# Optimization experiments

Measured on AMD Instinct MI355X. Metric: run time of the kernel, lower is better.

Reference implementation:

```python
import jax, jax.numpy as jnp
import numpy as np
from jax import lax

H, D_INNER, G, D_GATE, K, DH = 2560, 8192, 32, 4096, 4, 128
EPS = 1e-6


def setup_inputs() -> dict:
    key = jax.random.key(0)
    ks = jax.random.split(key, 9)
    B, L = 2, 4096
    s = 0.02
    return {
        "hidden_states": jax.random.normal(ks[0], (B, L, H), jnp.float32),
        "W_qkv": jax.random.normal(ks[1], (D_INNER, H), jnp.float32) * s,
        "W_b": jax.random.normal(ks[2], (G, H), jnp.float32) * s,
        "W_a": jax.random.normal(ks[3], (G, H), jnp.float32) * s,
        "conv_w": jax.random.normal(ks[4], (D_INNER, 1, K), jnp.float32) * s,
        "W_out": jax.random.normal(ks[5], (H, D_GATE), jnp.float32) * s,
        "norm_w": jnp.ones((DH,), jnp.float32),
        "A_log": jax.random.normal(ks[6], (G,), jnp.float32) * 0.1,
        "dt_bias": jax.random.normal(ks[7], (G,), jnp.float32) * 0.1,
    }


def _ssm_scan(x, B_coeff, C_coeff, A_log, dt_bias):
    # x: [B,L,G,DH], B_coeff/C_coeff: [B,L,G]
    A = -jnp.exp(A_log.astype(jnp.float32))          # [G]
    dt = jax.nn.softplus(dt_bias.astype(jnp.float32))  # [G]
    dA = jnp.exp(dt * A)                              # [G], time-invariant decay
    xf = x.astype(jnp.float32).transpose(1, 0, 2, 3)      # [L,B,G,DH]
    Bf = B_coeff.astype(jnp.float32).transpose(1, 0, 2)   # [L,B,G]
    Cf = C_coeff.astype(jnp.float32).transpose(1, 0, 2)
    h0 = jnp.zeros(x.shape[0:1] + (G, DH), jnp.float32)   # [B,G,DH]

    def step(h, inp):
        x_t, b_t, c_t = inp
        h = dA[None, :, None] * h + (dt * b_t)[..., None] * x_t
        return h, c_t[..., None] * h

    _, ys = lax.scan(step, h0, (xf, Bf, Cf))  # ys: [L,B,G,DH]
    return ys.transpose(1, 0, 2, 3).astype(x.dtype)


def reference(hidden_states, W_qkv, W_b, W_a, conv_w, W_out, norm_w, A_log, dt_bias):
    Bsz, L, _ = hidden_states.shape
    xz = hidden_states @ W_qkv.T           # [B,L,8192]
    B_coeff = hidden_states @ W_b.T        # [B,L,32]
    C_coeff = hidden_states @ W_a.T        # [B,L,32]
    # causal depthwise conv1d (padding K-1 on left, right pad trimmed)
    xz_c = lax.conv_general_dilated(
        xz.transpose(0, 2, 1), conv_w, (1,), [(K - 1, 0)],
        feature_group_count=D_INNER,
        dimension_numbers=("NCH", "OIH", "NCH"))
    xz_c = xz_c.transpose(0, 2, 1)          # [B,L,8192]
    x, z_inner = jnp.split(xz_c, 2, axis=-1)  # each [B,L,4096]
    x = jax.nn.silu(x).reshape(Bsz, L, G, DH)
    y = _ssm_scan(x, B_coeff, C_coeff, A_log, dt_bias)  # [B,L,G,DH]
    # RMSNorm over head_dim
    y = y * lax.rsqrt(jnp.mean(y * y, axis=-1, keepdims=True) + EPS) * norm_w
    y = y.reshape(Bsz, L, D_GATE) * jax.nn.silu(z_inner)
    return y @ W_out.T                      # [B,L,2560]
```

## Files before the change

### kernel.cpp

```cpp
#include <hip/hip_runtime.h>
#include <cstdint>
#include <cstddef>

#define H_DIM   2560
#define DINNER  8192
#define GHEADS  32
#define DGATE   4096
#define DH      128
#define BSZ     2
#define LSEQ    4096
#define MROWS   (BSZ*LSEQ)
#define NXPAD   4352
#define NCHUNK  64
#define SCHUNK  (LSEQ/NCHUNK)

typedef __attribute__((ext_vector_type(4))) float    f32x4;
typedef __attribute__((ext_vector_type(8))) _Float16 f16x8;
typedef unsigned short u16;
typedef unsigned int   u32;

static __device__ __forceinline__ u16 f2h(float f) {
  _Float16 h = (_Float16)f;
  union { _Float16 h; u16 u; } v; v.h = h; return v.u;
}
static __device__ __forceinline__ float h2f(u16 u) {
  union { u16 u; _Float16 h; } v; v.u = u; return (float)v.h;
}
static __device__ __forceinline__ float silu(float x) {
  return x / (1.0f + expf(-x));
}

__global__ void cast_f32_f16(const float* __restrict__ in, u16* __restrict__ out, int n4) {
  int i = blockIdx.x * blockDim.x + threadIdx.x;
  if (i < n4) {
    f32x4 v = ((const f32x4*)in)[i];
    u32 p0 = (u32)f2h(v[0]) | ((u32)f2h(v[1]) << 16);
    u32 p1 = (u32)f2h(v[2]) | ((u32)f2h(v[3]) << 16);
    ((uint2*)out)[i] = make_uint2(p0, p1);
  }
}

__global__ void build_wc(const float* __restrict__ Wqkv, const float* __restrict__ Wb,
                         const float* __restrict__ Wa, u16* __restrict__ wcp,
                         u16* __restrict__ wz) {
  int row = blockIdx.x;
  if (row >= NXPAD) {
    const float* src = Wqkv + (size_t)(4096 + row - NXPAD) * H_DIM;
    u16* oh = wz + (size_t)(row - NXPAD) * H_DIM;
    for (int i = threadIdx.x; i < H_DIM / 4; i += blockDim.x) {
      f32x4 v = ((const f32x4*)src)[i];
      ((uint2*)oh)[i] = make_uint2((u32)f2h(v[0]) | ((u32)f2h(v[1]) << 16),
                                   (u32)f2h(v[2]) | ((u32)f2h(v[3]) << 16));
    }
    return;
  }
  const float* src = nullptr;
  if (row < 4096)              src = Wqkv + (size_t)row * H_DIM;
  else if (row < 4128)         src = Wb + (size_t)(row - 4096) * H_DIM;
  else if (row < 4160)         src = Wa + (size_t)(row - 4128) * H_DIM;
  u16* oh = wcp + (size_t)row * H_DIM;
  for (int i = threadIdx.x; i < H_DIM / 4; i += blockDim.x) {
    u32 p0 = 0, p1 = 0;
    if (src) {
      f32x4 v = ((const f32x4*)src)[i];
      p0 = (u32)f2h(v[0]) | ((u32)f2h(v[1]) << 16);
      p1 = (u32)f2h(v[2]) | ((u32)f2h(v[3]) << 16);
    }
    ((uint2*)oh)[i] = make_uint2(p0, p1);
  }
}

static __device__ __forceinline__ void gload16(const u16* g, u16* l) {
  __builtin_amdgcn_global_load_lds(
      (const __attribute__((address_space(1))) u32*)g,
      (__attribute__((address_space(3))) u32*)l, 16, 0, 0);
}

#define BAR()    asm volatile("s_barrier" ::: "memory")
#define WAITV3() asm volatile("s_waitcnt vmcnt(3)" ::: "memory")
#define WAITV0() asm volatile("s_waitcnt vmcnt(0)" ::: "memory")

template<bool OUT_F16>
__global__ __launch_bounds__(512)
void gemm_h(const u16* __restrict__ A, const u16* __restrict__ Bt,
            void* __restrict__ Cout, int K, int ldc, int nbx, int cpx) {
  __shared__ __align__(16) u16 As0[128 * 32];
  __shared__ __align__(16) u16 As1[128 * 32];
  __shared__ __align__(16) u16 Bs0[256 * 32];
  __shared__ __align__(16) u16 Bs1[256 * 32];
  const int tid  = threadIdx.x;
  const int lane = tid & 63;
  const int wave = tid >> 6;
  const int wm = (wave & 1) * 64;
  const int wn = (wave >> 1) * 64;
  const int bid = blockIdx.x;
  const int lsw = (bid & 7) * cpx + (bid >> 3);
  const int by  = lsw / nbx;
  const int bx  = lsw - by * nbx;
  const size_t bm = (size_t)by * 128;
  const size_t bn = (size_t)bx * 256;

  const int srow = tid >> 2;
  const int scol = (((tid & 3) ^ ((srow >> 1) & 3)) << 3);
  const u16* Ab = A + bm * (size_t)K;
  const u16* Bb = Bt + bn * (size_t)K;

  f32x4 acc[4][4];
#pragma unroll
  for (int i = 0; i < 4; i++)
#pragma unroll
    for (int j = 0; j < 4; j++) acc[i][j] = (f32x4){0.f, 0.f, 0.f, 0.f};

#define STAGE(AS, BS, kk)                                                \
  do {                                                                   \
    gload16(Ab + (size_t)srow * K + (kk) + scol, &AS[tid * 8]);          \
    gload16(Bb + (size_t)srow * K + (kk) + scol, &BS[tid * 8]);          \
    gload16(Bb + (size_t)(128 + srow) * K + (kk) + scol, &BS[4096 + tid * 8]); \
  } while (0)

#define COMPUTE(AS, BS)                                                           \
  do {                                                                            \
    const int fr = lane & 15;                                                     \
    const int fo = (((lane >> 4) ^ ((fr >> 1) & 3)) << 3);    \
    f16x8 av[4], bv[4];                                                           \
    _Pragma("unroll")                                                             \
    for (int i = 0; i < 4; i++) av[i] = *(const f16x8*)&AS[(wm + i * 16 + fr) * 32 + fo]; \
    _Pragma("unroll")                                                             \
    for (int j = 0; j < 4; j++) bv[j] = *(const f16x8*)&BS[(wn + j * 16 + fr) * 32 + fo]; \
    __builtin_amdgcn_s_setprio(1);                                                \
    _Pragma("unroll")                                                             \
    for (int i = 0; i < 4; i++)                                                   \
      _Pragma("unroll")                                                           \
      for (int j = 0; j < 4; j++)                                                 \
        acc[i][j] = __builtin_amdgcn_mfma_f32_16x16x32_f16(av[i], bv[j], acc[i][j], 0, 0, 0); \
    __builtin_amdgcn_s_setprio(0);                                                \
  } while (0)

  STAGE(As0, Bs0, 0);
  STAGE(As1, Bs1, 32);
  WAITV3();
  BAR();
  for (int k0 = 0; k0 < K; k0 += 64) {
    COMPUTE(As0, Bs0);
    BAR();
    if (k0 + 64 < K) { STAGE(As0, Bs0, k0 + 64); WAITV3(); }
    else             { WAITV0(); }
    BAR();
    COMPUTE(As1, Bs1);
    BAR();
    if (k0 + 96 < K) { STAGE(As1, Bs1, k0 + 96); WAITV3(); }
    else             { WAITV0(); }
    BAR();
  }
#undef STAGE
#undef COMPUTE

  const int cr = (lane >> 4) * 4, ccol = lane & 15;
#pragma unroll
  for (int i = 0; i < 4; i++)
#pragma unroll
    for (int j = 0; j < 4; j++)
#pragma unroll
      for (int r = 0; r < 4; r++) {
        size_t row = bm + wm + i * 16 + cr + r;
        size_t col = bn + wn + j * 16 + ccol;
        if (OUT_F16) ((u16*)Cout)[row * ldc + col] = f2h(acc[i][j][r]);
        else         ((float*)Cout)[row * ldc + col] = acc[i][j][r];
      }
}

__global__ __launch_bounds__(64)
void scan_pass1(const float* __restrict__ xzx, const float* __restrict__ conv_w,
                const float* __restrict__ A_log, const float* __restrict__ dt_bias,
                float* __restrict__ E) {
  const int bid = blockIdx.x;
  const int c   = bid & (NCHUNK - 1);
  const int bg  = bid >> 6;
  const int g   = bg & (GHEADS - 1);
  const int b   = bg >> 5;
  const int lane = threadIdx.x;
  const int ch0 = g * DH + lane, ch1 = ch0 + 64;

  const f32x4 w0 = ((const f32x4*)conv_w)[ch0];
  const f32x4 w1 = ((const f32x4*)conv_w)[ch1];
  const float dt = log1pf(expf(dt_bias[g]));
  const float Ac = -expf(A_log[g]);
  const float dA = expf(dt * Ac);

  const int l0 = c * SCHUNK;
  const float* base = xzx + (size_t)b * LSEQ * NXPAD;

  float xm3 = 0, xm2 = 0, xm1 = 0, Xm3 = 0, Xm2 = 0, Xm1 = 0;
#pragma unroll
  for (int j = 0; j < 3; j++) {
    int l = l0 - 3 + j;
    float v0 = 0, v1 = 0;
    if (l >= 0) {
      const float* rp = base + (size_t)l * NXPAD;
      v0 = rp[ch0]; v1 = rp[ch1];
    }
    if (j == 0) { xm3 = v0; Xm3 = v1; }
    else if (j == 1) { xm2 = v0; Xm2 = v1; }
    else { xm1 = v0; Xm1 = v1; }
  }
  float h0 = 0.f, h1 = 0.f;
  for (int t = 0; t < SCHUNK; t++) {
    const float* rp = base + (size_t)(l0 + t) * NXPAD;
    float xc0 = rp[ch0], xc1 = rp[ch1];
    float cx0 = w0[0] * xm3 + w0[1] * xm2 + w0[2] * xm1 + w0[3] * xc0;
    float cx1 = w1[0] * Xm3 + w1[1] * Xm2 + w1[2] * Xm1 + w1[3] * xc1;
    xm3 = xm2; xm2 = xm1; xm1 = xc0;
    Xm3 = Xm2; Xm2 = Xm1; Xm1 = xc1;
    float u = dt * rp[DGATE + g];
    h0 = dA * h0 + u * silu(cx0);
    h1 = dA * h1 + u * silu(cx1);
  }
  float* ep = E + (size_t)bid * DH;
  ep[lane] = h0; ep[lane + 64] = h1;
}

__global__ __launch_bounds__(64)
void scan_pass2(const float* __restrict__ E, float* __restrict__ Hs,
                const float* __restrict__ A_log, const float* __restrict__ dt_bias) {
  const int bg = blockIdx.x;
  const int g = bg & (GHEADS - 1);
  const int lane = threadIdx.x;
  const float dt = log1pf(expf(dt_bias[g]));
  const float Ac = -expf(A_log[g]);
  const float dAS = expf(dt * Ac * (float)SCHUNK);
  float h0 = 0.f, h1 = 0.f;
  for (int c = 0; c < NCHUNK; c++) {
    size_t idx = ((size_t)bg * NCHUNK + c) * DH;
    Hs[idx + lane] = h0; Hs[idx + lane + 64] = h1;
    h0 = dAS * h0 + E[idx + lane];
    h1 = dAS * h1 + E[idx + lane + 64];
  }
}

__global__ __launch_bounds__(64)
void scan_pass3(const float* __restrict__ xzx, const u16* __restrict__ xzz,
                const float* __restrict__ conv_w,
                const float* __restrict__ A_log, const float* __restrict__ dt_bias,
                const float* __restrict__ norm_w, const float* __restrict__ Hs,
                u16* __restrict__ gbuf) {
  const int bid = blockIdx.x;
  const int c   = bid & (NCHUNK - 1);
  const int bg  = bid >> 6;
  const int g   = bg & (GHEADS - 1);
  const int b   = bg >> 5;
  const int lane = threadIdx.x;
  const int ch0 = g * DH + lane, ch1 = ch0 + 64;

  const f32x4 wx0 = ((const f32x4*)conv_w)[ch0];
  const f32x4 wx1 = ((const f32x4*)conv_w)[ch1];
  const f32x4 wz0 = ((const f32x4*)conv_w)[DGATE + ch0];
  const f32x4 wz1 = ((const f32x4*)conv_w)[DGATE + ch1];
  const float nw0 = norm_w[lane], nw1 = norm_w[lane + 64];

  const float dt = log1pf(expf(dt_bias[g]));
  const float Ac = -expf(A_log[g]);
  const float dA = expf(dt * Ac);

  const int l0 = c * SCHUNK;
  const float* basex = xzx + (size_t)b * LSEQ * NXPAD;
  const u16*   basez = xzz + (size_t)b * LSEQ * DGATE;

  float xm3 = 0, xm2 = 0, xm1 = 0, Xm3 = 0, Xm2 = 0, Xm1 = 0;
  float zm3 = 0, zm2 = 0, zm1 = 0, Zm3 = 0, Zm2 = 0, Zm1 = 0;
#pragma unroll
  for (int j = 0; j < 3; j++) {
    int l = l0 - 3 + j;
    float vx0 = 0, vx1 = 0, vz0 = 0, vz1 = 0;
    if (l >= 0) {
      const float* rp = basex + (size_t)l * NXPAD;
      const u16*   rz = basez + (size_t)l * DGATE;
      vx0 = rp[ch0]; vx1 = rp[ch1];
      vz0 = h2f(rz[ch0]); vz1 = h2f(rz[ch1]);
    }
    if (j == 0) { xm3 = vx0; Xm3 = vx1; zm3 = vz0; Zm3 = vz1; }
    else if (j == 1) { xm2 = vx0; Xm2 = vx1; zm2 = vz0; Zm2 = vz1; }
    else { xm1 = vx0; Xm1 = vx1; zm1 = vz0; Zm1 = vz1; }
  }
  float h0 = Hs[(size_t)bid * DH + lane];
  float h1 = Hs[(size_t)bid * DH + lane + 64];
  for (int t = 0; t < SCHUNK; t++) {
    const int l = l0 + t;
    const float* rp = basex + (size_t)l * NXPAD;
    const u16*   rz = basez + (size_t)l * DGATE;
    float xc0 = rp[ch0], xc1 = rp[ch1];
    float zc0 = h2f(rz[ch0]), zc1 = h2f(rz[ch1]);
    float cx0 = wx0[0] * xm3 + wx0[1] * xm2 + wx0[2] * xm1 + wx0[3] * xc0;
    float cx1 = wx1[0] * Xm3 + wx1[1] * Xm2 + wx1[2] * Xm1 + wx1[3] * xc1;
    float cz0 = wz0[0] * zm3 + wz0[1] * zm2 + wz0[2] * zm1 + wz0[3] * zc0;
    float cz1 = wz1[0] * Zm3 + wz1[1] * Zm2 + wz1[2] * Zm1 + wz1[3] * zc1;
    xm3 = xm2; xm2 = xm1; xm1 = xc0;  Xm3 = Xm2; Xm2 = Xm1; Xm1 = xc1;
    zm3 = zm2; zm2 = zm1; zm1 = zc0;  Zm3 = Zm2; Zm2 = Zm1; Zm1 = zc1;
    float bcl = rp[DGATE + g];
    float ccl = rp[DGATE + 32 + g];
    float u = dt * bcl;
    h0 = dA * h0 + u * silu(cx0);
    h1 = dA * h1 + u * silu(cx1);
    float y0 = ccl * h0, y1 = ccl * h1;
    float ss = y0 * y0 + y1 * y1;
    ss += __shfl_xor(ss, 32); ss += __shfl_xor(ss, 16); ss += __shfl_xor(ss, 8);
    ss += __shfl_xor(ss, 4);  ss += __shfl_xor(ss, 2);  ss += __shfl_xor(ss, 1);
    const float sc = rsqrtf(ss * (1.0f / DH) + 1e-6f);
    u16* op = gbuf + (size_t)(b * LSEQ + l) * DGATE + g * DH;
    op[lane]      = f2h(y0 * sc * nw0 * silu(cz0));
    op[lane + 64] = f2h(y1 * sc * nw1 * silu(cz1));
  }
}

extern "C" void kernel_launch(void* const* d_in, const int* in_sizes, int n_in,
                              void* d_out, int out_size, void* d_ws, size_t ws_size,
                              hipStream_t stream) {
  (void)in_sizes; (void)n_in; (void)out_size; (void)ws_size;
  const float* hs    = (const float*)d_in[0];
  const float* Wqkv  = (const float*)d_in[1];
  const float* Wb    = (const float*)d_in[2];
  const float* Wa    = (const float*)d_in[3];
  const float* convw = (const float*)d_in[4];
  const float* Wout  = (const float*)d_in[5];
  const float* normw = (const float*)d_in[6];
  const float* Alog  = (const float*)d_in[7];
  const float* dtb   = (const float*)d_in[8];
  float* out = (float*)d_out;

  char* ws = (char*)d_ws;
  size_t off = 0;
  auto alloc = [&](size_t bytes) { void* p = ws + off; off += (bytes + 255) & ~(size_t)255; return p; };
  float* xzx    = (float*)alloc((size_t)MROWS * NXPAD * 4);
  u16*   xzz    = (u16*)alloc((size_t)MROWS * DGATE * 2);
  u16*   wcp    = (u16*)alloc((size_t)NXPAD * H_DIM * 2);
  u16*   wz     = (u16*)alloc((size_t)DGATE * H_DIM * 2);
  (void)alloc((size_t)24 << 20);
  u16*   wout_h = (u16*)alloc((size_t)H_DIM * DGATE * 2);
  float* E      = (float*)alloc((size_t)BSZ * GHEADS * NCHUNK * DH * 4);
  float* Hst    = (float*)alloc((size_t)BSZ * GHEADS * NCHUNK * DH * 4);
  u16*   gbuf   = wcp;
  u16*   hs_h   = (u16*)d_out;

  const int n4_hs = MROWS * H_DIM / 4;
  cast_f32_f16<<<(n4_hs + 255) / 256, 256, 0, stream>>>(hs, hs_h, n4_hs);
  build_wc<<<NXPAD + DGATE, 256, 0, stream>>>(Wqkv, Wb, Wa, wcp, wz);
  const int n4_wo = H_DIM * DGATE / 4;
  cast_f32_f16<<<(n4_wo + 255) / 256, 256, 0, stream>>>(Wout, wout_h, n4_wo);

  gemm_h<false><<<1088, 512, 0, stream>>>(hs_h, wcp, xzx, H_DIM, NXPAD, 17, 136);
  gemm_h<true><<<1024, 512, 0, stream>>>(hs_h, wz, xzz, H_DIM, DGATE, 16, 128);

  scan_pass1<<<BSZ * GHEADS * NCHUNK, 64, 0, stream>>>(xzx, convw, Alog, dtb, E);
  scan_pass2<<<BSZ * GHEADS, 64, 0, stream>>>(E, Hst, Alog, dtb);
  scan_pass3<<<BSZ * GHEADS * NCHUNK, 64, 0, stream>>>(xzx, xzz, convw, Alog, dtb, normw, Hst, gbuf);

  gemm_h<false><<<640, 512, 0, stream>>>(gbuf, wout_h, out, DGATE, H_DIM, 10, 80);
}
```

Before: 854.5 us.

## Merge input GEMMs into one launch with triple-buffered LDS pipeline

Concatenates the xz and z weight matrices into one combined fp16 buffer so the two input projection GEMMs run as a single launch, with each tile choosing an f32 or f16 output by column block. The GEMM mainloop moves from double to triple buffering of LDS stages, waiting on vmcnt(6) so more loads are in flight. The tile mapping is changed to column-major over 64 row blocks, and launch bounds now request 4 waves per SIMD. The cost is more LDS per block (72KB), which may reduce occupancy, and tail handling that assumes particular K multiples.

Result: slower. 1.482 ms (+73.4%).

```diff
diff --git a/kernel.cpp b/kernel.cpp
--- a/kernel.cpp
+++ b/kernel.cpp
@@ -11,6 +11,7 @@
 #define LSEQ    4096
 #define MROWS   (BSZ*LSEQ)
 #define NXPAD   4352
+#define NWCOMB  8448
 #define NCHUNK  64
 #define SCHUNK  (LSEQ/NCHUNK)
 
@@ -41,24 +42,14 @@
 }
 
 __global__ void build_wc(const float* __restrict__ Wqkv, const float* __restrict__ Wb,
-                         const float* __restrict__ Wa, u16* __restrict__ wcp,
-                         u16* __restrict__ wz) {
+                         const float* __restrict__ Wa, u16* __restrict__ wcomb) {
   int row = blockIdx.x;
-  if (row >= NXPAD) {
-    const float* src = Wqkv + (size_t)(4096 + row - NXPAD) * H_DIM;
-    u16* oh = wz + (size_t)(row - NXPAD) * H_DIM;
-    for (int i = threadIdx.x; i < H_DIM / 4; i += blockDim.x) {
-      f32x4 v = ((const f32x4*)src)[i];
-      ((uint2*)oh)[i] = make_uint2((u32)f2h(v[0]) | ((u32)f2h(v[1]) << 16),
-                                   (u32)f2h(v[2]) | ((u32)f2h(v[3]) << 16));
-    }
-    return;
-  }
   const float* src = nullptr;
   if (row < 4096)              src = Wqkv + (size_t)row * H_DIM;
   else if (row < 4128)         src = Wb + (size_t)(row - 4096) * H_DIM;
   else if (row < 4160)         src = Wa + (size_t)(row - 4128) * H_DIM;
-  u16* oh = wcp + (size_t)row * H_DIM;
+  else if (row >= NXPAD)       src = Wqkv + (size_t)(4096 + row - NXPAD) * H_DIM;
+  u16* oh = wcomb + (size_t)row * H_DIM;
   for (int i = threadIdx.x; i < H_DIM / 4; i += blockDim.x) {
     u32 p0 = 0, p1 = 0;
     if (src) {
@@ -77,33 +68,36 @@
 }
 
 #define BAR()    asm volatile("s_barrier" ::: "memory")
+#define WAITV6() asm volatile("s_waitcnt vmcnt(6)" ::: "memory")
 #define WAITV3() asm volatile("s_waitcnt vmcnt(3)" ::: "memory")
 #define WAITV0() asm volatile("s_waitcnt vmcnt(0)" ::: "memory")
 
-template<bool OUT_F16>
-__global__ __launch_bounds__(512)
-void gemm_h(const u16* __restrict__ A, const u16* __restrict__ Bt,
-            void* __restrict__ Cout, int K, int ldc, int nbx, int cpx) {
+__global__ __launch_bounds__(512, 4)
+void gemm3(const u16* __restrict__ A, const u16* __restrict__ Bt,
+           float* __restrict__ Cf32, u16* __restrict__ Cf16,
+           int K, int ldc32, int ldc16, int nbx, int nf32) {
   __shared__ __align__(16) u16 As0[128 * 32];
   __shared__ __align__(16) u16 As1[128 * 32];
+  __shared__ __align__(16) u16 As2[128 * 32];
   __shared__ __align__(16) u16 Bs0[256 * 32];
   __shared__ __align__(16) u16 Bs1[256 * 32];
+  __shared__ __align__(16) u16 Bs2[256 * 32];
   const int tid  = threadIdx.x;
   const int lane = tid & 63;
   const int wave = tid >> 6;
   const int wm = (wave & 1) * 64;
   const int wn = (wave >> 1) * 64;
   const int bid = blockIdx.x;
+  const int cpx = nbx << 3;
   const int lsw = (bid & 7) * cpx + (bid >> 3);
-  const int by  = lsw / nbx;
-  const int bx  = lsw - by * nbx;
+  const int bx  = lsw >> 6;
+  const int by  = lsw & 63;
   const size_t bm = (size_t)by * 128;
-  const size_t bn = (size_t)bx * 256;
+  const u16* Ab = A  + bm * (size_t)K;
+  const u16* Bb = Bt + (size_t)bx * 256 * K;
 
   const int srow = tid >> 2;
   const int scol = (((tid & 3) ^ ((srow >> 1) & 3)) << 3);
-  const u16* Ab = A + bm * (size_t)K;
-  const u16* Bb = Bt + bn * (size_t)K;
 
   f32x4 acc[4][4];
 #pragma unroll
@@ -136,37 +130,57 @@
     __builtin_amdgcn_s_setprio(0);                                                \
   } while (0)
 
+  const int S = K >> 5;
   STAGE(As0, Bs0, 0);
   STAGE(As1, Bs1, 32);
-  WAITV3();
+  STAGE(As2, Bs2, 64);
+  WAITV6();
   BAR();
-  for (int k0 = 0; k0 < K; k0 += 64) {
-    COMPUTE(As0, Bs0);
-    BAR();
-    if (k0 + 64 < K) { STAGE(As0, Bs0, k0 + 64); WAITV3(); }
-    else             { WAITV0(); }
-    BAR();
-    COMPUTE(As1, Bs1);
-    BAR();
-    if (k0 + 96 < K) { STAGE(As1, Bs1, k0 + 96); WAITV3(); }
-    else             { WAITV0(); }
-    BAR();
-  }
+  int i = 0;
+  for (; i + 3 < S; i += 3) {
+    COMPUTE(As0, Bs0); BAR();
+    STAGE(As0, Bs0, (i + 3) * 32);
+    WAITV6(); BAR();
+    COMPUTE(As1, Bs1); BAR();
+    if (i + 4 < S) STAGE(As1, Bs1, (i + 4) * 32);
+    WAITV6(); BAR();
+    COMPUTE(As2, Bs2); BAR();
+    if (i + 5 < S) STAGE(As2, Bs2, (i + 5) * 32);
+    WAITV6(); BAR();
+  }
+  WAITV3(); BAR();
+  COMPUTE(As0, Bs0);
+  if (S - i >= 2) { WAITV0(); BAR(); COMPUTE(As1, Bs1); }
+  if (S - i >= 3) { COMPUTE(As2, Bs2); }
 #undef STAGE
 #undef COMPUTE
 
   const int cr = (lane >> 4) * 4, ccol = lane & 15;
-#pragma unroll
-  for (int i = 0; i < 4; i++)
-#pragma unroll
-    for (int j = 0; j < 4; j++)
-#pragma unroll
-      for (int r = 0; r < 4; r++) {
-        size_t row = bm + wm + i * 16 + cr + r;
-        size_t col = bn + wn + j * 16 + ccol;
-        if (OUT_F16) ((u16*)Cout)[row * ldc + col] = f2h(acc[i][j][r]);
-        else         ((float*)Cout)[row * ldc + col] = acc[i][j][r];
-      }
+  if (bx < nf32) {
+    const size_t cb = (size_t)bx * 256;
+#pragma unroll
+    for (int i2 = 0; i2 < 4; i2++)
+#pragma unroll
+      for (int j = 0; j < 4; j++)
+#pragma unroll
+        for (int r = 0; r < 4; r++) {
+          size_t row = bm + wm + i2 * 16 + cr + r;
+          size_t col = cb + wn + j * 16 + ccol;
+          Cf32[row * ldc32 + col] = acc[i2][j][r];
+        }
+  } else {
+    const size_t cb = (size_t)(bx - nf32) * 256;
+#pragma unroll
+    for (int i2 = 0; i2 < 4; i2++)
+#pragma unroll
+      for (int j = 0; j < 4; j++)
+#pragma unroll
+        for (int r = 0; r < 4; r++) {
+          size_t row = bm + wm + i2 * 16 + cr + r;
+          size_t col = cb + wn + j * 16 + ccol;
+          Cf16[row * ldc16 + col] = f2h(acc[i2][j][r]);
+        }
+  }
 }
 
 __global__ __launch_bounds__(64)
@@ -331,27 +345,25 @@
   auto alloc = [&](size_t bytes) { void* p = ws + off; off += (bytes + 255) & ~(size_t)255; return p; };
   float* xzx    = (float*)alloc((size_t)MROWS * NXPAD * 4);
   u16*   xzz    = (u16*)alloc((size_t)MROWS * DGATE * 2);
-  u16*   wcp    = (u16*)alloc((size_t)NXPAD * H_DIM * 2);
-  u16*   wz     = (u16*)alloc((size_t)DGATE * H_DIM * 2);
+  u16*   wcomb  = (u16*)alloc((size_t)NWCOMB * H_DIM * 2);
   (void)alloc((size_t)24 << 20);
   u16*   wout_h = (u16*)alloc((size_t)H_DIM * DGATE * 2);
   float* E      = (float*)alloc((size_t)BSZ * GHEADS * NCHUNK * DH * 4);
   float* Hst    = (float*)alloc((size_t)BSZ * GHEADS * NCHUNK * DH * 4);
-  u16*   gbuf   = wcp;
+  u16*   gbuf   = wcomb;
   u16*   hs_h   = (u16*)d_out;
 
   const int n4_hs = MROWS * H_DIM / 4;
   cast_f32_f16<<<(n4_hs + 255) / 256, 256, 0, stream>>>(hs, hs_h, n4_hs);
-  build_wc<<<NXPAD + DGATE, 256, 0, stream>>>(Wqkv, Wb, Wa, wcp, wz);
+  build_wc<<<NWCOMB, 256, 0, stream>>>(Wqkv, Wb, Wa, wcomb);
   const int n4_wo = H_DIM * DGATE / 4;
   cast_f32_f16<<<(n4_wo + 255) / 256, 256, 0, stream>>>(Wout, wout_h, n4_wo);
 
-  gemm_h<false><<<1088, 512, 0, stream>>>(hs_h, wcp, xzx, H_DIM, NXPAD, 17, 136);
-  gemm_h<true><<<1024, 512, 0, stream>>>(hs_h, wz, xzz, H_DIM, DGATE, 16, 128);
+  gemm3<<<33 * 64, 512, 0, stream>>>(hs_h, wcomb, xzx, xzz, H_DIM, NXPAD, DGATE, 33, 17);
 
   scan_pass1<<<BSZ * GHEADS * NCHUNK, 64, 0, stream>>>(xzx, convw, Alog, dtb, E);
   scan_pass2<<<BSZ * GHEADS, 64, 0, stream>>>(E, Hst, Alog, dtb);
   scan_pass3<<<BSZ * GHEADS * NCHUNK, 64, 0, stream>>>(xzx, xzz, convw, Alog, dtb, normw, Hst, gbuf);
 
-  gemm_h<false><<<640, 512, 0, stream>>>(gbuf, wout_h, out, DGATE, H_DIM, 10, 80);
-}
+  gemm3<<<10 * 64, 512, 0, stream>>>(gbuf, wout_h, out, nullptr, DGATE, H_DIM, 0, 10, 10);
+}
```
